# Kernel tuning notes

Measured on AMD Instinct MI355X. Metric: run time of the kernel, lower is better.

Reference implementation:

```python
import jax, jax.numpy as jnp
import numpy as np

B, N, F_IN = 32, 512, 64
HEADS = (8, 8)
HIDS = (64, 64)
EDGE_P = 0.05  # graph density
NEG_SLOPE = 0.2
NEG_INF = -1e20


def setup_inputs() -> dict:
    key = jax.random.key(0)
    ks = jax.random.split(key, 8)
    x = jax.random.normal(ks[0], (B, N, F_IN), dtype=jnp.float32)
    adj = (jax.random.uniform(ks[1], (B, N, N)) < EDGE_P).astype(jnp.float32)
    adj = jnp.maximum(adj, adj.transpose(0, 2, 1))  # symmetric adjacency
    # mask = (batch, row): every (b, n) pair gets the masked softmax
    b_idx = jnp.repeat(jnp.arange(B, dtype=jnp.int32), N)   # [B*N]
    r_idx = jnp.tile(jnp.arange(N, dtype=jnp.int32), B)     # [B*N]
    # layer 0: f_in=64 -> f_out=64, H=8 ; layer 1: f_in=64*8=512 -> f_out=64, H=8
    W0 = jax.random.normal(ks[2], (F_IN, HIDS[0]), dtype=jnp.float32) / jnp.sqrt(jnp.float32(F_IN))
    a_src0 = jax.random.normal(ks[3], (HIDS[0], HEADS[0]), dtype=jnp.float32) / jnp.sqrt(jnp.float32(HIDS[0]))
    a_dst0 = jax.random.normal(ks[4], (HIDS[0], HEADS[0]), dtype=jnp.float32) / jnp.sqrt(jnp.float32(HIDS[0]))
    f_in1 = HIDS[0] * HEADS[0]
    W1 = jax.random.normal(ks[5], (f_in1, HIDS[1]), dtype=jnp.float32) / jnp.sqrt(jnp.float32(f_in1))
    a_src1 = jax.random.normal(ks[6], (HIDS[1], HEADS[1]), dtype=jnp.float32) / jnp.sqrt(jnp.float32(HIDS[1]))
    a_dst1 = jax.random.normal(ks[7], (HIDS[1], HEADS[1]), dtype=jnp.float32) / jnp.sqrt(jnp.float32(HIDS[1]))
    return dict(x=x, adj=adj, b_idx=b_idx, r_idx=r_idx,
                W0=W0, a_src0=a_src0, a_dst0=a_dst0,
                W1=W1, a_src1=a_src1, a_dst1=a_dst1)


def _gat_layer(x, adj, b_idx, r_idx, W, a_src, a_dst):
    # x: [B,N,f_in], adj: [B,N,N] (diag already set), W: [f_in,F], a_*: [F,H]
    hp = x @ W                                        # [B,N,F]
    s = jnp.einsum('bnf,fh->bhn', hp, a_src)          # attn_src
    d = jnp.einsum('bnf,fh->bhn', hp, a_dst)          # attn_dst
    attn = s[:, :, :, None] + d[:, :, None, :]        # [B,H,N,N]
    attn = jnp.where(attn >= 0, attn, NEG_SLOPE * attn)  # leaky_relu(0.2)
    attn = jnp.where(adj[:, None, :, :] == 0, 0.0, attn)  # masked_fill(adj==0, 0)
    rows = attn[b_idx, :, r_idx, :]                   # [K,H,N]
    rows = jnp.where(rows == 0.0, NEG_INF, rows)
    rows = jax.nn.softmax(rows, axis=-1)
    attn = attn.at[b_idx, :, r_idx, :].set(rows)
    return jnp.einsum('bhij,bjf->bhif', attn, hp)     # [B,H,N,F]


def reference(x, adj, b_idx, r_idx, W0, a_src0, a_dst0, W1, a_src1, a_dst1):
    Bn, Nn = x.shape[:2]
    # torch mutates adj in place: adj[batch,row,row] = 1 (self loops)
    adj = adj.at[b_idx, r_idx, r_idx].set(1.0)
    o = _gat_layer(x, adj, b_idx, r_idx, W0, a_src0, a_dst0)      # [B,H,N,F0]
    x1 = jax.nn.elu(o.transpose(0, 2, 1, 3).reshape(Bn, Nn, -1))  # [B,N,H*F0]
    o2 = _gat_layer(x1, adj, b_idx, r_idx, W1, a_src1, a_dst1)    # [B,H,N,F1]
    return o2.mean(axis=1)                                        # [B,N,F1]
```

## Files before the change

### kernel.cpp

```cpp
#include <hip/hip_runtime.h>
#include <hip/hip_bf16.h>
#include <math.h>

#define BB 32
#define NN 512

typedef _Float16 f16x8 __attribute__((ext_vector_type(8)));
typedef __fp16  fp16x2 __attribute__((ext_vector_type(2)));
typedef float f32x4 __attribute__((ext_vector_type(4)));

#define MFMA16(a, b, c) __builtin_amdgcn_mfma_f32_16x16x32_f16(a, b, c, 0, 0, 0)

union AF { f16x8 v; unsigned int u[4]; };

__device__ __forceinline__ void gload_lds16(const void* g, void* l) {
    __builtin_amdgcn_global_load_lds(
        (const __attribute__((address_space(1))) unsigned int*)g,
        (__attribute__((address_space(3))) unsigned int*)l, 16, 0, 0);
}
__device__ __forceinline__ void gload_lds4(const void* g, void* l) {
    __builtin_amdgcn_global_load_lds(
        (const __attribute__((address_space(1))) unsigned int*)g,
        (__attribute__((address_space(3))) unsigned int*)l, 4, 0, 0);
}

__device__ __forceinline__ unsigned fenc(float f) {
    unsigned b = __float_as_uint(f);
    return (b & 0x80000000u) ? ~b : (b | 0x80000000u);
}
__device__ __forceinline__ float fdec(unsigned u) {
    return __uint_as_float((u & 0x80000000u) ? (u ^ 0x80000000u) : ~u);
}

__global__ __launch_bounds__(256) void k_wt_prep(
    const float* __restrict__ W0, _Float16* __restrict__ W0T,
    const float* __restrict__ W1, _Float16* __restrict__ W1T,
    unsigned* __restrict__ maxdz)
{
    int id = blockIdx.x * 256 + threadIdx.x;
    if (id < 512) maxdz[id] = 0u;
    const float* W; _Float16* WT; int KT, task;
    if (id < 512) { W = W0; WT = W0T; KT = 64;  task = id; }
    else          { W = W1; WT = W1T; KT = 512; task = id - 512; }
    int n = task & 63, gabs = task >> 6;
    int c = gabs >> 3, g = gabs & 7;
    f16x8 hv;
#pragma unroll
    for (int e = 0; e < 8; ++e)
        hv[e] = (_Float16)W[(size_t)(gabs * 8 + e) * 64 + n];
    *(f16x8*)(WT + (size_t)n * KT + c * 64 + (g ^ (n & 7)) * 8) = hv;
}

static __device__ __forceinline__ void epi_sd_hpt(
    const float* ctile, const float* asd_f, int row0, int t,
    float* __restrict__ s, float* __restrict__ dTg, _Float16* __restrict__ hpT,
    float* dmax_lds, unsigned* __restrict__ maxd_out)
{
    int b = row0 >> 9, jb = row0 & 511;
    if (t < 128) {
        int rr = t >> 3, h = t & 7;
        float sv = 0.f, dv = 0.f;
#pragma unroll
        for (int f = 0; f < 64; ++f) {
            float hv = ctile[rr * 66 + f];
            sv = fmaf(hv, asd_f[f * 8 + h], sv);
            dv = fmaf(hv, asd_f[512 + f * 8 + h], dv);
        }
        s[((size_t)b * NN + jb + rr) * 8 + h] = sv;
        dTg[((size_t)b * 8 + h) * NN + jb + rr] = dv;
        dmax_lds[t] = dv;
    } else if (t < 256) {
        int t2 = t - 128;
        int f = t2 >> 1, jl = (t2 & 1) * 8;
        f16x8 hv;
#pragma unroll
        for (int e = 0; e < 8; ++e)
            hv[e] = (_Float16)ctile[(jl + e) * 66 + f];
        *(f16x8*)(hpT + ((size_t)b * 64 + f) * NN + jb + jl) = hv;
    }
    __syncthreads();
    if (t < 8) {
        float m = dmax_lds[t];
#pragma unroll
        for (int k = 1; k < 16; ++k) m = fmaxf(m, dmax_lds[t + 8 * k]);
        atomicMax(maxd_out + (b * 8 + t), fenc(m));
    }
}

__global__ __launch_bounds__(256) void k_gemm0(
    const float* __restrict__ x, const _Float16* __restrict__ W0T,
    const float* __restrict__ a_src, const float* __restrict__ a_dst,
    const float* __restrict__ adj, unsigned long long* __restrict__ adjb,
    float* __restrict__ s, float* __restrict__ dTg, _Float16* __restrict__ hpT,
    unsigned* __restrict__ maxd)
{
    __shared__ float ctile[16 * 66];
    __shared__ float asd_f[1024];
    __shared__ unsigned int mrow[16][16];
    __shared__ float dmax[128];
    int t = threadIdx.x, row0 = blockIdx.x * 16;
    int lane = t & 63, w = t >> 6, cn = lane & 15, rq = lane >> 4;

    int ar = t >> 4, seg = t & 15;
    const float* ap = adj + (size_t)(row0 + ar) * NN + seg * 32;
    float4 av[8];
#pragma unroll
    for (int q = 0; q < 8; ++q) av[q] = ((const float4*)ap)[q];

    ((float4*)asd_f)[t] = (t < 128) ? ((const float4*)a_src)[t]
                                    : ((const float4*)a_dst)[t - 128];
    f32x4 acc;
#pragma unroll
    for (int e = 0; e < 4; ++e) acc[e] = 0.f;
#pragma unroll
    for (int ks = 0; ks < 2; ++ks) {
        const float* xp = x + (size_t)(row0 + cn) * 64 + ks * 32 + rq * 8;
        float4 x0 = *(const float4*)xp, x1 = *(const float4*)(xp + 4);
        f16x8 ah = {(_Float16)x0.x, (_Float16)x0.y, (_Float16)x0.z, (_Float16)x0.w,
                    (_Float16)x1.x, (_Float16)x1.y, (_Float16)x1.z, (_Float16)x1.w};
        int nn = w * 16 + cn;
        f16x8 bh = *(const f16x8*)(W0T + (size_t)nn * 64 + (((ks * 4 + rq) ^ (nn & 7)) * 8));
        acc = MFMA16(ah, bh, acc);
    }
#pragma unroll
    for (int r = 0; r < 4; ++r)
        ctile[(rq * 4 + r) * 66 + w * 16 + cn] = acc[r];
    __syncthreads();
    epi_sd_hpt(ctile, asd_f, row0, t, s, dTg, hpT, dmax, maxd);

    unsigned int m32 = 0;
#pragma unroll
    for (int q = 0; q < 8; ++q) {
        if (av[q].x != 0.f) m32 |= 1u << (q * 4 + 0);
        if (av[q].y != 0.f) m32 |= 1u << (q * 4 + 1);
        if (av[q].z != 0.f) m32 |= 1u << (q * 4 + 2);
        if (av[q].w != 0.f) m32 |= 1u << (q * 4 + 3);
    }
    int i = (row0 + ar) & (NN - 1);
    if ((i >> 5) == seg) m32 |= 1u << (i & 31);
    mrow[ar][seg] = m32;
    __syncthreads();
    if (t < 128) {
        int r = t >> 3, k = t & 7;
        unsigned long long u = (unsigned long long)mrow[r][2 * k]
                             | ((unsigned long long)mrow[r][2 * k + 1] << 32);
        adjb[(size_t)(row0 + r) * 8 + k] = u;
    }
}

#define PSTEP(DDv, MBYTE, KS, HTC)                                      \
    do {                                                                \
        AF aA;                                                          \
        _Pragma("unroll")                                               \
        for (int e = 0; e < 8; e += 2) {                                \
            float pA[2];                                                \
            _Pragma("unroll")                                           \
            for (int q = 0; q < 2; ++q) {                               \
                int ee = e + q;                                         \
                bool con = (MBYTE >> ee) & 1u;                          \
                float e0 = sv + DDv[ee];                                \
                float l0 = fmaxf(e0, 0.2f * e0);                        \
                float p0 = __expf(l0 - M);                              \
                pA[q] = (con && l0 != 0.f) ? p0 : 0.f;                  \
            }                                                           \
            fp16x2 ka = __builtin_amdgcn_cvt_pkrtz(pA[0], pA[1]);       \
            aA.u[e >> 1] = __builtin_bit_cast(unsigned int, ka);        \
        }                                                               \
        accrs = MFMA16(aA.v, ones, accrs);                              \
        _Pragma("unroll")                                               \
        for (int ft = 0; ft < 4; ++ft) {                                \
            int f = ft * 16 + cn;                                       \
            f16x8 bh = *(const f16x8*)&HTC[f * 64 + ((((KS) * 4 + rq) ^ (f & 7)) * 8)]; \
            acc[ft] = MFMA16(aA.v, bh, acc[ft]);                        \
        }                                                               \
    } while (0)

template<int MODE>
__global__ __launch_bounds__(512, 8) void k_attn_fused(
    const unsigned long long* __restrict__ adjb, const float* __restrict__ s,
    const float* __restrict__ dTg, const unsigned* __restrict__ maxd,
    const _Float16* __restrict__ hpT,
    const _Float16* __restrict__ W1T,
    const float* __restrict__ a_src, const float* __restrict__ a_dst,
    float* __restrict__ s_out, float* __restrict__ dTg_out,
    _Float16* __restrict__ hpT_out, unsigned* __restrict__ maxd_out,
    float* __restrict__ o_f)
{
    __shared__ __align__(16) char smem[20480];
    char* bufP = smem;
    char* bufQ = smem + 10240;

    int blk = blockIdx.x;
    int vb = ((blk & 7) << 7) | (blk >> 3);
    int b = vb >> 5, i0 = (vb & 31) << 4;
    int row0 = vb * 16;
    int t = threadIdx.x, lane = t & 63, w = t >> 6;
    int cn = lane & 15, rq = lane >> 4;
    int myrow = i0 + cn;

    const _Float16* hb = hpT + (size_t)b * 64 * NN;
    int f0 = t >> 3, g0 = t & 7;
    const _Float16* hsrc = hb + (size_t)f0 * NN + ((g0 ^ (f0 & 7)) * 8);
    const float* dsrc = dTg + ((size_t)b * 8 + w) * NN + lane;

    {
        gload_lds16(hsrc, (_Float16*)bufP + (w << 9));
        gload_lds4(dsrc, (float*)(bufP + 8192) + (w << 6));
    }

    float sv = s[((size_t)b * NN + myrow) * 8 + w];
    float md = fdec(maxd[b * 8 + w]);
    float M = fmaxf(sv + md, 0.f);
    const unsigned long long* abr = adjb + ((size_t)b * NN + myrow) * 8;
    int rq8 = rq * 8;

    f16x8 ones;
#pragma unroll
    for (int e = 0; e < 8; ++e) ones[e] = (_Float16)1.0f;

    f32x4 acc[4], accrs;
#pragma unroll
    for (int e = 0; e < 4; ++e) accrs[e] = 0.f;
#pragma unroll
    for (int ft = 0; ft < 4; ++ft)
#pragma unroll
        for (int e = 0; e < 4; ++e) acc[ft][e] = 0.f;

    unsigned long long mb = abr[0];
    __syncthreads();

    for (int jcx = 0; jcx < 8; ++jcx) {
        int jc = jcx * 64;
        char* cur = (jcx & 1) ? bufQ : bufP;
        char* nxt = (jcx & 1) ? bufP : bufQ;
        if (jcx < 7) {
            gload_lds16(hsrc + jc + 64, (_Float16*)nxt + (w << 9));
            gload_lds4(dsrc + jc + 64, (float*)(nxt + 8192) + (w << 6));
        }
        unsigned long long mbn = (jcx < 7) ? abr[jcx + 1] : 0ull;
        const _Float16* hTc = (const _Float16*)cur;
        const float* ddl = (const float*)(cur + 8192) + (w << 6);
        unsigned int ml = (unsigned int)mb, mh = (unsigned int)(mb >> 32);
#pragma unroll
        for (int ks = 0; ks < 2; ++ks) {
            float dd[8];
            *(float4*)&dd[0] = *(const float4*)(ddl + ks * 32 + rq8);
            *(float4*)&dd[4] = *(const float4*)(ddl + ks * 32 + rq8 + 4);
            unsigned int mby = ((ks ? mh : ml) >> rq8) & 0xffu;
            PSTEP(dd, mby, ks, hTc);
        }
        mb = mbn;
        __syncthreads();
    }

    float invr[4];
#pragma unroll
    for (int r = 0; r < 4; ++r) invr[r] = 1.0f / accrs[r];

    if (MODE == 0) {
        _Float16* x1all = (_Float16*)smem;
#pragma unroll
        for (int ft = 0; ft < 4; ++ft)
#pragma unroll
            for (int r = 0; r < 4; ++r) {
                int il = rq * 4 + r;
                float v = acc[ft][r] * invr[r];
                v = v > 0.f ? v : __expf(v) - 1.f;
                int f = ft * 16 + cn;
                x1all[w * 1024 + il * 64 + (((f >> 3) ^ (il & 7)) * 8) + (f & 7)] =
                    (_Float16)v;
            }
        __syncthreads();
        f32x4 g1;
#pragma unroll
        for (int e = 0; e < 4; ++e) g1[e] = 0.f;
        int nn = (w & 3) * 16 + cn, kh = w >> 2;
        const _Float16* wb = W1T + (size_t)nn * 512;
#pragma unroll
        for (int kc2 = 0; kc2 < 4; ++kc2) {
            int kc = kh * 4 + kc2;
#pragma unroll
            for (int ks = 0; ks < 2; ++ks) {
                f16x8 ah = *(const f16x8*)&x1all[kc * 1024 + cn * 64 +
                                                 (((ks * 4 + rq) ^ (cn & 7)) * 8)];
                f16x8 bh = *(const f16x8*)(wb + kc * 64 +
                                           (((ks * 4 + rq) ^ (nn & 7)) * 8));
                g1 = MFMA16(ah, bh, g1);
            }
        }
        __syncthreads();
        float* ct = (float*)smem;
        float* asd_f = (float*)(smem + 12288);
        float* dmax = (float*)(smem + 16384);
#pragma unroll
        for (int r = 0; r < 4; ++r)
            ct[kh * 1056 + (rq * 4 + r) * 66 + nn] = g1[r];
        if (t < 256)
            ((float4*)asd_f)[t] = (t < 128) ? ((const float4*)a_src)[t]
                                            : ((const float4*)a_dst)[t - 128];
        __syncthreads();
        for (int idx = t; idx < 1056; idx += 512) ct[idx] += ct[1056 + idx];
        __syncthreads();
        epi_sd_hpt(ct, asd_f, row0, t, s_out, dTg_out, hpT_out, dmax, maxd_out);
    } else {
        float* red = (float*)smem;
#pragma unroll
        for (int ph = 0; ph < 2; ++ph) {
            if ((w >> 2) == ph) {
#pragma unroll
                for (int ft = 0; ft < 4; ++ft)
#pragma unroll
                    for (int r = 0; r < 4; ++r) {
                        int il = rq * 4 + r;
                        float v = acc[ft][r] * invr[r];
                        int off = (w & 3) * 1024 + il * 64 + ft * 16 + cn;
                        if (ph == 0) red[off] = v;
                        else         red[off] += v;
                    }
            }
            __syncthreads();
        }
#pragma unroll
        for (int u = 0; u < 2; ++u) {
            int idx = t + u * 512;
            int il = idx >> 6, f = idx & 63;
            float sum = red[il * 64 + f] + red[1024 + il * 64 + f]
                      + red[2048 + il * 64 + f] + red[3072 + il * 64 + f];
            o_f[((size_t)b * NN + i0 + il) * 64 + f] = sum * 0.125f;
        }
    }
}

extern "C" void kernel_launch(void* const* d_in, const int* in_sizes, int n_in,
                              void* d_out, int out_size, void* d_ws, size_t ws_size,
                              hipStream_t stream) {
    const float* x      = (const float*)d_in[0];
    const float* adj    = (const float*)d_in[1];
    const float* W0     = (const float*)d_in[4];
    const float* a_src0 = (const float*)d_in[5];
    const float* a_dst0 = (const float*)d_in[6];
    const float* W1     = (const float*)d_in[7];
    const float* a_src1 = (const float*)d_in[8];
    const float* a_dst1 = (const float*)d_in[9];
    float* out = (float*)d_out;

    float* ws = (float*)d_ws;
    const size_t R = (size_t)BB * NN;
    const size_t BHN = (size_t)BB * 8 * NN;
    float* s0    = ws;
    float* dTg0  = s0 + R * 8;
    float* s1    = dTg0 + BHN;
    float* dTg1  = s1 + R * 8;
    unsigned* maxd0 = (unsigned*)(dTg1 + BHN);
    unsigned* maxd1 = maxd0 + 256;
    _Float16* hp0T = (_Float16*)(maxd1 + 256);
    _Float16* hp1T = hp0T + (size_t)BB * 64 * NN;
    _Float16* W0T  = hp1T + (size_t)BB * 64 * NN;
    _Float16* W1T  = W0T + (size_t)64 * 64;
    unsigned long long* adjb = (unsigned long long*)(W1T + (size_t)64 * 512);

    k_wt_prep<<<18, 256, 0, stream>>>(W0, W0T, W1, W1T, maxd0);
    k_gemm0<<<1024, 256, 0, stream>>>(x, W0T, a_src0, a_dst0, adj, adjb,
                                      s0, dTg0, hp0T, maxd0);
    k_attn_fused<0><<<1024, 512, 0, stream>>>(adjb, s0, dTg0, maxd0, hp0T,
                                              W1T, a_src1, a_dst1,
                                              s1, dTg1, hp1T, maxd1, nullptr);
    k_attn_fused<1><<<1024, 512, 0, stream>>>(adjb, s1, dTg1, maxd1, hp1T,
                                              nullptr, nullptr, nullptr,
                                              nullptr, nullptr, nullptr, nullptr, out);
}
```

Baseline: 160.0 us.

## Process 32 rows per attention block to reuse staged hp and d tiles

Each attention block now covers 32 query rows (two 16-row MFMA tiles) instead of 16, so the staged hpT and dst tiles in LDS serve twice as many rows. Grid size halves to 512 blocks, launch bounds drop to 4 waves per SIMD, and LDS grows to about 38KB. The aim is to halve the global/LDS traffic for the key-side data per output row. The cost is more registers and LDS per block and fewer blocks, which lowers occupancy and parallelism on 256 CUs.

Measured after the change: 160.7 us. About the same (+0.5%).

```diff
diff --git a/kernel.cpp b/kernel.cpp
--- a/kernel.cpp
+++ b/kernel.cpp
@@ -51,7 +51,7 @@
     *(f16x8*)(WT + (size_t)n * KT + c * 64 + (g ^ (n & 7)) * 8) = hv;
 }
 
-static __device__ __forceinline__ void epi_sd_hpt(
+static __device__ __forceinline__ void epi16(
     const float* ctile, const float* asd_f, int row0, int t,
     float* __restrict__ s, float* __restrict__ dTg, _Float16* __restrict__ hpT,
     float* dmax_lds, unsigned* __restrict__ maxd_out)
@@ -83,6 +83,42 @@
         float m = dmax_lds[t];
 #pragma unroll
         for (int k = 1; k < 16; ++k) m = fmaxf(m, dmax_lds[t + 8 * k]);
+        atomicMax(maxd_out + (b * 8 + t), fenc(m));
+    }
+}
+
+static __device__ __forceinline__ void epi32(
+    const float* ctile, const float* asd_f, int row0, int t,
+    float* __restrict__ s, float* __restrict__ dTg, _Float16* __restrict__ hpT,
+    float* dmax_lds, unsigned* __restrict__ maxd_out)
+{
+    int b = row0 >> 9, jb = row0 & 511;
+    if (t < 256) {
+        int rr = t >> 3, h = t & 7;
+        float sv = 0.f, dv = 0.f;
+#pragma unroll
+        for (int f = 0; f < 64; ++f) {
+            float hv = ctile[rr * 66 + f];
+            sv = fmaf(hv, asd_f[f * 8 + h], sv);
+            dv = fmaf(hv, asd_f[512 + f * 8 + h], dv);
+        }
+        s[((size_t)b * NN + jb + rr) * 8 + h] = sv;
+        dTg[((size_t)b * 8 + h) * NN + jb + rr] = dv;
+        dmax_lds[t] = dv;
+    } else {
+        int t2 = t - 256;
+        int f = t2 >> 2, jl = (t2 & 3) * 8;
+        f16x8 hv;
+#pragma unroll
+        for (int e = 0; e < 8; ++e)
+            hv[e] = (_Float16)ctile[(jl + e) * 66 + f];
+        *(f16x8*)(hpT + ((size_t)b * 64 + f) * NN + jb + jl) = hv;
+    }
+    __syncthreads();
+    if (t < 8) {
+        float m = dmax_lds[t];
+#pragma unroll
+        for (int k = 1; k < 32; ++k) m = fmaxf(m, dmax_lds[t + 8 * k]);
         atomicMax(maxd_out + (b * 8 + t), fenc(m));
     }
 }
@@ -126,7 +162,7 @@
     for (int r = 0; r < 4; ++r)
         ctile[(rq * 4 + r) * 66 + w * 16 + cn] = acc[r];
     __syncthreads();
-    epi_sd_hpt(ctile, asd_f, row0, t, s, dTg, hpT, dmax, maxd);
+    epi16(ctile, asd_f, row0, t, s, dTg, hpT, dmax, maxd);
 
     unsigned int m32 = 0;
 #pragma unroll
@@ -148,9 +184,8 @@
     }
 }
 
-#define PSTEP(DDv, MBYTE, KS, HTC)                                      \
+#define PBUILD(AOUT, SV, M_, MBYTE, DDv)                                \
     do {                                                                \
-        AF aA;                                                          \
         _Pragma("unroll")                                               \
         for (int e = 0; e < 8; e += 2) {                                \
             float pA[2];                                                \
@@ -158,25 +193,18 @@
             for (int q = 0; q < 2; ++q) {                               \
                 int ee = e + q;                                         \
                 bool con = (MBYTE >> ee) & 1u;                          \
-                float e0 = sv + DDv[ee];                                \
+                float e0 = SV + DDv[ee];                                \
                 float l0 = fmaxf(e0, 0.2f * e0);                        \
-                float p0 = __expf(l0 - M);                              \
+                float p0 = __expf(l0 - M_);                             \
                 pA[q] = (con && l0 != 0.f) ? p0 : 0.f;                  \
             }                                                           \
             fp16x2 ka = __builtin_amdgcn_cvt_pkrtz(pA[0], pA[1]);       \
-            aA.u[e >> 1] = __builtin_bit_cast(unsigned int, ka);        \
-        }                                                               \
-        accrs = MFMA16(aA.v, ones, accrs);                              \
-        _Pragma("unroll")                                               \
-        for (int ft = 0; ft < 4; ++ft) {                                \
-            int f = ft * 16 + cn;                                       \
-            f16x8 bh = *(const f16x8*)&HTC[f * 64 + ((((KS) * 4 + rq) ^ (f & 7)) * 8)]; \
-            acc[ft] = MFMA16(aA.v, bh, acc[ft]);                        \
+            AOUT.u[e >> 1] = __builtin_bit_cast(unsigned int, ka);      \
         }                                                               \
     } while (0)
 
 template<int MODE>
-__global__ __launch_bounds__(512, 8) void k_attn_fused(
+__global__ __launch_bounds__(512, 4) void k_attn_fused(
     const unsigned long long* __restrict__ adjb, const float* __restrict__ s,
     const float* __restrict__ dTg, const unsigned* __restrict__ maxd,
     const _Float16* __restrict__ hpT,
@@ -186,14 +214,14 @@
     _Float16* __restrict__ hpT_out, unsigned* __restrict__ maxd_out,
     float* __restrict__ o_f)
 {
-    __shared__ __align__(16) char smem[20480];
+    __shared__ __align__(16) char smem[38400];
     char* bufP = smem;
     char* bufQ = smem + 10240;
 
     int blk = blockIdx.x;
-    int vb = ((blk & 7) << 7) | (blk >> 3);
-    int b = vb >> 5, i0 = (vb & 31) << 4;
-    int row0 = vb * 16;
+    int vb = ((blk & 7) << 6) | (blk >> 3);
+    int b = vb >> 4, i0 = (vb & 15) << 5;
+    int row0 = vb * 32;
     int t = threadIdx.x, lane = t & 63, w = t >> 6;
     int cn = lane & 15, rq = lane >> 4;
     int myrow = i0 + cn;
@@ -208,9 +236,11 @@
         gload_lds4(dsrc, (float*)(bufP + 8192) + (w << 6));
     }
 
-    float sv = s[((size_t)b * NN + myrow) * 8 + w];
+    float svA = s[((size_t)b * NN + myrow) * 8 + w];
+    float svB = s[((size_t)b * NN + myrow + 16) * 8 + w];
     float md = fdec(maxd[b * 8 + w]);
-    float M = fmaxf(sv + md, 0.f);
+    float MA = fmaxf(svA + md, 0.f);
+    float MB = fmaxf(svB + md, 0.f);
     const unsigned long long* abr = adjb + ((size_t)b * NN + myrow) * 8;
     int rq8 = rq * 8;
 
@@ -218,15 +248,15 @@
 #pragma unroll
     for (int e = 0; e < 8; ++e) ones[e] = (_Float16)1.0f;
 
-    f32x4 acc[4], accrs;
-#pragma unroll
-    for (int e = 0; e < 4; ++e) accrs[e] = 0.f;
+    f32x4 accA[4], accB[4], accrsA, accrsB;
+#pragma unroll
+    for (int e = 0; e < 4; ++e) { accrsA[e] = 0.f; accrsB[e] = 0.f; }
 #pragma unroll
     for (int ft = 0; ft < 4; ++ft)
 #pragma unroll
-        for (int e = 0; e < 4; ++e) acc[ft][e] = 0.f;
-
-    unsigned long long mb = abr[0];
+        for (int e = 0; e < 4; ++e) { accA[ft][e] = 0.f; accB[ft][e] = 0.f; }
+
+    unsigned long long mbA = abr[0], mbB = abr[128];
     __syncthreads();
 
     for (int jcx = 0; jcx < 8; ++jcx) {
@@ -237,43 +267,63 @@
             gload_lds16(hsrc + jc + 64, (_Float16*)nxt + (w << 9));
             gload_lds4(dsrc + jc + 64, (float*)(nxt + 8192) + (w << 6));
         }
-        unsigned long long mbn = (jcx < 7) ? abr[jcx + 1] : 0ull;
+        unsigned long long mbnA = (jcx < 7) ? abr[jcx + 1] : 0ull;
+        unsigned long long mbnB = (jcx < 7) ? abr[jcx + 129] : 0ull;
         const _Float16* hTc = (const _Float16*)cur;
         const float* ddl = (const float*)(cur + 8192) + (w << 6);
-        unsigned int ml = (unsigned int)mb, mh = (unsigned int)(mb >> 32);
+        unsigned int mlA = (unsigned)mbA, mhA = (unsigned)(mbA >> 32);
+        unsigned int mlB = (unsigned)mbB, mhB = (unsigned)(mbB >> 32);
 #pragma unroll
         for (int ks = 0; ks < 2; ++ks) {
             float dd[8];
             *(float4*)&dd[0] = *(const float4*)(ddl + ks * 32 + rq8);
             *(float4*)&dd[4] = *(const float4*)(ddl + ks * 32 + rq8 + 4);
-            unsigned int mby = ((ks ? mh : ml) >> rq8) & 0xffu;
-            PSTEP(dd, mby, ks, hTc);
-        }
-        mb = mbn;
+            unsigned int mbyA = ((ks ? mhA : mlA) >> rq8) & 0xffu;
+            unsigned int mbyB = ((ks ? mhB : mlB) >> rq8) & 0xffu;
+            AF aA, aB;
+            PBUILD(aA, svA, MA, mbyA, dd);
+            PBUILD(aB, svB, MB, mbyB, dd);
+            accrsA = MFMA16(aA.v, ones, accrsA);
+            accrsB = MFMA16(aB.v, ones, accrsB);
+#pragma unroll
+            for (int ft = 0; ft < 4; ++ft) {
+                int f = ft * 16 + cn;
+                f16x8 bh = *(const f16x8*)&hTc[f * 64 + (((ks * 4 + rq) ^ (f & 7)) * 8)];
+                accA[ft] = MFMA16(aA.v, bh, accA[ft]);
+                accB[ft] = MFMA16(aB.v, bh, accB[ft]);
+            }
+        }
+        mbA = mbnA; mbB = mbnB;
         __syncthreads();
     }
 
-    float invr[4];
-#pragma unroll
-    for (int r = 0; r < 4; ++r) invr[r] = 1.0f / accrs[r];
+    float invrA[4], invrB[4];
+#pragma unroll
+    for (int r = 0; r < 4; ++r) {
+        invrA[r] = 1.0f / accrsA[r];
+        invrB[r] = 1.0f / accrsB[r];
+    }
 
     if (MODE == 0) {
         _Float16* x1all = (_Float16*)smem;
 #pragma unroll
-        for (int ft = 0; ft < 4; ++ft)
-#pragma unroll
-            for (int r = 0; r < 4; ++r) {
-                int il = rq * 4 + r;
-                float v = acc[ft][r] * invr[r];
-                v = v > 0.f ? v : __expf(v) - 1.f;
-                int f = ft * 16 + cn;
-                x1all[w * 1024 + il * 64 + (((f >> 3) ^ (il & 7)) * 8) + (f & 7)] =
-                    (_Float16)v;
-            }
+        for (int rt = 0; rt < 2; ++rt)
+#pragma unroll
+            for (int ft = 0; ft < 4; ++ft)
+#pragma unroll
+                for (int r = 0; r < 4; ++r) {
+                    int il = rt * 16 + rq * 4 + r;
+                    float v = rt ? accB[ft][r] * invrB[r]
+                                 : accA[ft][r] * invrA[r];
+                    v = v > 0.f ? v : __expf(v) - 1.f;
+                    int f = ft * 16 + cn;
+                    x1all[w * 2048 + il * 64 + (((f >> 3) ^ (il & 7)) * 8) + (f & 7)] =
+                        (_Float16)v;
+                }
         __syncthreads();
-        f32x4 g1;
-#pragma unroll
-        for (int e = 0; e < 4; ++e) g1[e] = 0.f;
+        f32x4 g1A, g1B;
+#pragma unroll
+        for (int e = 0; e < 4; ++e) { g1A[e] = 0.f; g1B[e] = 0.f; }
         int nn = (w & 3) * 16 + cn, kh = w >> 2;
         const _Float16* wb = W1T + (size_t)nn * 512;
 #pragma unroll
@@ -281,51 +331,59 @@
             int kc = kh * 4 + kc2;
 #pragma unroll
             for (int ks = 0; ks < 2; ++ks) {
-                f16x8 ah = *(const f16x8*)&x1all[kc * 1024 + cn * 64 +
-                                                 (((ks * 4 + rq) ^ (cn & 7)) * 8)];
                 f16x8 bh = *(const f16x8*)(wb + kc * 64 +
                                            (((ks * 4 + rq) ^ (nn & 7)) * 8));
-                g1 = MFMA16(ah, bh, g1);
+                f16x8 ahA = *(const f16x8*)&x1all[kc * 2048 + cn * 64 +
+                                                  (((ks * 4 + rq) ^ (cn & 7)) * 8)];
+                f16x8 ahB = *(const f16x8*)&x1all[kc * 2048 + (16 + cn) * 64 +
+                                                  (((ks * 4 + rq) ^ (cn & 7)) * 8)];
+                g1A = MFMA16(ahA, bh, g1A);
+                g1B = MFMA16(ahB, bh, g1B);
             }
         }
         __syncthreads();
         float* ct = (float*)smem;
-        float* asd_f = (float*)(smem + 12288);
-        float* dmax = (float*)(smem + 16384);
-#pragma unroll
-        for (int r = 0; r < 4; ++r)
-            ct[kh * 1056 + (rq * 4 + r) * 66 + nn] = g1[r];
+        float* asd_f = (float*)(smem + 33280);
+        float* dmax = (float*)(smem + 37376);
+#pragma unroll
+        for (int r = 0; r < 4; ++r) {
+            ct[kh * 2112 + (rq * 4 + r) * 66 + nn] = g1A[r];
+            ct[kh * 2112 + (16 + rq * 4 + r) * 66 + nn] = g1B[r];
+        }
         if (t < 256)
             ((float4*)asd_f)[t] = (t < 128) ? ((const float4*)a_src)[t]
                                             : ((const float4*)a_dst)[t - 128];
         __syncthreads();
-        for (int idx = t; idx < 1056; idx += 512) ct[idx] += ct[1056 + idx];
+        for (int idx = t; idx < 2112; idx += 512) ct[idx] += ct[2112 + idx];
         __syncthreads();
-        epi_sd_hpt(ct, asd_f, row0, t, s_out, dTg_out, hpT_out, dmax, maxd_out);
+        epi32(ct, asd_f, row0, t, s_out, dTg_out, hpT_out, dmax, maxd_out);
     } else {
         float* red = (float*)smem;
 #pragma unroll
         for (int ph = 0; ph < 2; ++ph) {
             if ((w >> 2) == ph) {
 #pragma unroll
-                for (int ft = 0; ft < 4; ++ft)
-#pragma unroll
-                    for (int r = 0; r < 4; ++r) {
-                        int il = rq * 4 + r;
-                        float v = acc[ft][r] * invr[r];
-                        int off = (w & 3) * 1024 + il * 64 + ft * 16 + cn;
-                        if (ph == 0) red[off] = v;
-                        else         red[off] += v;
-                    }
+                for (int rt = 0; rt < 2; ++rt)
+#pragma unroll
+                    for (int ft = 0; ft < 4; ++ft)
+#pragma unroll
+                        for (int r = 0; r < 4; ++r) {
+                            int il = rt * 16 + rq * 4 + r;
+                            float v = rt ? accB[ft][r] * invrB[r]
+                                         : accA[ft][r] * invrA[r];
+                            int off = (w & 3) * 2048 + il * 64 + ft * 16 + cn;
+                            if (ph == 0) red[off] = v;
+                            else         red[off] += v;
+                        }
             }
             __syncthreads();
         }
 #pragma unroll
-        for (int u = 0; u < 2; ++u) {
+        for (int u = 0; u < 4; ++u) {
             int idx = t + u * 512;
             int il = idx >> 6, f = idx & 63;
-            float sum = red[il * 64 + f] + red[1024 + il * 64 + f]
-                      + red[2048 + il * 64 + f] + red[3072 + il * 64 + f];
+            float sum = red[il * 64 + f] + red[2048 + il * 64 + f]
+                      + red[4096 + il * 64 + f] + red[6144 + il * 64 + f];
             o_f[((size_t)b * NN + i0 + il) * 64 + f] = sum * 0.125f;
         }
     }
@@ -362,10 +420,10 @@
     k_wt_prep<<<18, 256, 0, stream>>>(W0, W0T, W1, W1T, maxd0);
     k_gemm0<<<1024, 256, 0, stream>>>(x, W0T, a_src0, a_dst0, adj, adjb,
                                       s0, dTg0, hp0T, maxd0);
-    k_attn_fused<0><<<1024, 512, 0, stream>>>(adjb, s0, dTg0, maxd0, hp0T,
-                                              W1T, a_src1, a_dst1,
-                                              s1, dTg1, hp1T, maxd1, nullptr);
-    k_attn_fused<1><<<1024, 512, 0, stream>>>(adjb, s1, dTg1, maxd1, hp1T,
-                                              nullptr, nullptr, nullptr,
-                                              nullptr, nullptr, nullptr, nullptr, out);
-}
+    k_attn_fused<0><<<512, 512, 0, stream>>>(adjb, s0, dTg0, maxd0, hp0T,
+                                             W1T, a_src1, a_dst1,
+                                             s1, dTg1, hp1T, maxd1, nullptr);
+    k_attn_fused<1><<<512, 512, 0, stream>>>(adjb, s1, dTg1, maxd1, hp1T,
+                                             nullptr, nullptr, nullptr,
+                                             nullptr, nullptr, nullptr, nullptr, out);
+}
```
